# Kernel optimization log

Measured on AMD Instinct MI355X. Metric: run time of the kernel, lower is better.

## Reference

```python
import jax, jax.numpy as jnp
import numpy as np

G, FO, FI = 8, 64, 64   # n_group, fo, fi
N_ITER = 3
B, H, W = 32, 64, 64


def setup_inputs() -> dict:
    key = jax.random.key(0)
    k1, k2, k3 = jax.random.split(key, 3)
    x = jax.random.normal(k1, (B, G * FI, H, W), jnp.float32)
    # kaiming_normal on [fo*g, fi, 1, 1] -> std = sqrt(2/fi); stored as [g, fo, fi]
    weight = jax.random.normal(k2, (G, FO, FI), jnp.float32) * np.float32(np.sqrt(2.0 / FI))
    bias = jax.random.normal(k3, (FO,), jnp.float32)
    return {"x": x, "weight": weight, "bias": bias}


def reference(x, weight, bias):
    b, c, h, w = x.shape
    g, fo, fi = weight.shape
    # grouped 1x1 conv: split channels into g groups of fi, contract each with its [fo, fi] block
    xr = x.reshape(b, g, fi, h, w)
    con = jnp.einsum('bgihw,goi->bgohw', xr, weight)  # [B, g, fo, H, W]
    beta = jnp.zeros((1, g, 1, 1, 1), dtype=x.dtype)
    for i in range(N_ITER):
        alpha = jax.nn.sigmoid(beta)
        v = jnp.sum(alpha * con, axis=1, keepdims=True)      # [B, 1, fo, H, W]
        if i == N_ITER - 1:
            return v[:, 0] + bias[None, :, None, None]       # [B, fo, H, W]
        beta = beta + jnp.sum(v * con, axis=2, keepdims=True)  # [B, g, 1, H, W]
```

## Files before the change

### kernel.cpp

```cpp
#include <hip/hip_runtime.h>


#define NG 8
#define NFO 64
#define NFI 64
#define NB 32
#define NH 64
#define NW 64
#define HW (NH * NW)

typedef float v2f __attribute__((ext_vector_type(2)));

__device__ __forceinline__ void stage_piece(const float* gsrc, float* ldst) {
    __builtin_amdgcn_global_load_lds(
        (const __attribute__((address_space(1))) void*)gsrc,
        (__attribute__((address_space(3))) void*)ldst, 16, 0, 0);
}

__global__ __launch_bounds__(256) void dynrout_kernel(
    const float* __restrict__ x, const float* __restrict__ weight,
    const float* __restrict__ bias, float* __restrict__ out)
{
    const int tid = threadIdx.x;
    const int p = tid & 63;
    const int q = __builtin_amdgcn_readfirstlane(tid >> 6);

    const int wg = blockIdx.x;
    const int b = wg >> 6;
    const int h = wg & 63;

    __shared__ __align__(16) float smem[6144];

    const float* xrow = x + (size_t)b * (NG * NFI) * HW + (size_t)h * NW;
    const float* gpiece = xrow + (size_t)(p >> 4) * HW + (size_t)(p & 15) * 4;

    float con[8][16];
#pragma unroll
    for (int g = 0; g < 8; ++g)
#pragma unroll
        for (int f = 0; f < 16; ++f) con[g][f] = 0.f;

#pragma unroll
    for (int cc = 0; cc < 2; ++cc) {
        float* dst = smem + cc * 2048;
        const float* g0 = gpiece + (size_t)(cc * 32) * HW;
        stage_piece(g0 + (size_t)(q * 8) * HW,     dst + (q * 2) * 256);
        stage_piece(g0 + (size_t)(q * 8 + 4) * HW, dst + (q * 2 + 1) * 256);
    }

#pragma unroll
    for (int c = 0; c < 16; ++c) {
        if (c < 15) asm volatile("s_waitcnt vmcnt(2)" ::: "memory");
        else        asm volatile("s_waitcnt vmcnt(0)" ::: "memory");
        __builtin_amdgcn_s_barrier();

        if (c < 14) {
            float* dst = smem + ((c + 2) % 3) * 2048;
            const float* g0 = gpiece + (size_t)((c + 2) * 32) * HW;
            stage_piece(g0 + (size_t)(q * 8) * HW,     dst + (q * 2) * 256);
            stage_piece(g0 + (size_t)(q * 8 + 4) * HW, dst + (q * 2 + 1) * 256);
        }

        const int g = c >> 1;
        const float* bufp = smem + (c % 3) * 2048;

        v2f xp[16];
#pragma unroll
        for (int jp = 0; jp < 16; ++jp) {
            xp[jp].x = bufp[(2 * jp) * 64 + p];
            xp[jp].y = bufp[(2 * jp + 1) * 64 + p];
        }

        const float* wq = weight + ((size_t)g * NFO + (size_t)q * 16) * NFI + (c & 1) * 32;
#pragma unroll
        for (int f = 0; f < 16; ++f) {
            const float* wr = wq + (size_t)f * NFI;
            v2f a0 = {0.f, 0.f}, a1 = {0.f, 0.f};
#pragma unroll
            for (int jp = 0; jp < 16; jp += 2) {
                const v2f w0 = *(const v2f*)(wr + 2 * jp);
                const v2f w1 = *(const v2f*)(wr + 2 * jp + 2);
                a0 = __builtin_elementwise_fma(w0, xp[jp], a0);
                a1 = __builtin_elementwise_fma(w1, xp[jp + 1], a1);
            }
            con[g][f] += (a0.x + a1.x) + (a0.y + a1.y);
        }
    }
    __syncthreads();

    float* pbuf   = smem;
    float* alphaS = smem + 2048;
    float* betaS  = smem + 2560;

    float v[16];

#pragma unroll
    for (int f = 0; f < 16; ++f) {
        float s = con[0][f];
#pragma unroll
        for (int g = 1; g < 8; ++g) s += con[g][f];
        v[f] = 0.5f * s;
    }
#pragma unroll
    for (int g = 0; g < 8; ++g) {
        float s = 0.f;
#pragma unroll
        for (int f = 0; f < 16; ++f) s = fmaf(v[f], con[g][f], s);
        pbuf[(q * 8 + g) * 64 + p] = s;
    }
    __syncthreads();
    for (int k = tid; k < 512; k += 256) {
        const int gg = k >> 6, pp = k & 63;
        const float bs = pbuf[gg * 64 + pp] + pbuf[512 + gg * 64 + pp] +
                         pbuf[1024 + gg * 64 + pp] + pbuf[1536 + gg * 64 + pp];
        betaS[gg * 64 + pp] = bs;
        alphaS[gg * 64 + pp] = 1.f / (1.f + __expf(-bs));
    }
    __syncthreads();

    float a[8];
#pragma unroll
    for (int g = 0; g < 8; ++g) a[g] = alphaS[g * 64 + p];
#pragma unroll
    for (int f = 0; f < 16; ++f) {
        float s = 0.f;
#pragma unroll
        for (int g = 0; g < 8; ++g) s = fmaf(a[g], con[g][f], s);
        v[f] = s;
    }
#pragma unroll
    for (int g = 0; g < 8; ++g) {
        float s = 0.f;
#pragma unroll
        for (int f = 0; f < 16; ++f) s = fmaf(v[f], con[g][f], s);
        pbuf[(q * 8 + g) * 64 + p] = s;
    }
    __syncthreads();
    for (int k = tid; k < 512; k += 256) {
        const int gg = k >> 6, pp = k & 63;
        const float bs = betaS[gg * 64 + pp] +
                         pbuf[gg * 64 + pp] + pbuf[512 + gg * 64 + pp] +
                         pbuf[1024 + gg * 64 + pp] + pbuf[1536 + gg * 64 + pp];
        alphaS[gg * 64 + pp] = 1.f / (1.f + __expf(-bs));
    }
    __syncthreads();

#pragma unroll
    for (int g = 0; g < 8; ++g) a[g] = alphaS[g * 64 + p];

    const float* bq = bias + q * 16;
    float* orow = out + (((size_t)b * NFO + (size_t)q * 16) * NH + h) * NW + p;
#pragma unroll
    for (int f = 0; f < 16; ++f) {
        float s = bq[f];
#pragma unroll
        for (int g = 0; g < 8; ++g) s = fmaf(a[g], con[g][f], s);
        orow[(size_t)f * HW] = s;
    }
}

extern "C" void kernel_launch(void* const* d_in, const int* in_sizes, int n_in,
                              void* d_out, int out_size, void* d_ws, size_t ws_size,
                              hipStream_t stream) {
    const float* x      = (const float*)d_in[0];
    const float* weight = (const float*)d_in[1];
    const float* bias   = (const float*)d_in[2];
    float* out = (float*)d_out;

    dynrout_kernel<<<dim3(NB * NH), dim3(256), 0, stream>>>(x, weight, bias, out);
}
```

Before: 564.1 us.

## Split fused kernel into grouped-conv kernel and routing kernel via workspace

```diff
diff --git a/kernel.cpp b/kernel.cpp
--- a/kernel.cpp
+++ b/kernel.cpp
@@ -17,6 +17,155 @@
         (__attribute__((address_space(3))) void*)ldst, 16, 0, 0);
 }
 
+__global__ __launch_bounds__(256, 8) void conv_kernel(
+    const float* __restrict__ x, const float* __restrict__ weight,
+    float* __restrict__ con)
+{
+    const int tid = threadIdx.x;
+    const int p = tid & 63;
+    const int q = __builtin_amdgcn_readfirstlane(tid >> 6);
+
+    const int id = blockIdx.x;
+    const int t = id & 63;
+    const int g = (id >> 6) & 7;
+    const int b = id >> 9;
+
+    __shared__ __align__(16) float smem[4096];
+
+    const float* xg = x + ((size_t)b * (NG * NFI) + (size_t)g * NFI) * HW + t * 64;
+
+#pragma unroll
+    for (int cc = 0; cc < 4; ++cc) {
+        const int chb = q * 16 + cc * 4;
+        stage_piece(xg + (size_t)(chb + (p >> 4)) * HW + (p & 15) * 4,
+                    smem + chb * 64);
+    }
+    asm volatile("s_waitcnt vmcnt(0)" ::: "memory");
+    __builtin_amdgcn_s_barrier();
+
+    v2f acc[16];
+#pragma unroll
+    for (int f = 0; f < 16; ++f) acc[f] = (v2f){0.f, 0.f};
+
+    const float* wq = weight + ((size_t)g * NFO + (size_t)q * 16) * NFI;
+#pragma unroll
+    for (int ib = 0; ib < 8; ++ib) {
+        v2f xq[4];
+#pragma unroll
+        for (int j = 0; j < 4; ++j) {
+            xq[j].x = smem[(ib * 8 + 2 * j) * 64 + p];
+            xq[j].y = smem[(ib * 8 + 2 * j + 1) * 64 + p];
+        }
+#pragma unroll
+        for (int f = 0; f < 16; ++f) {
+            const float* wr = wq + (size_t)f * NFI + ib * 8;
+#pragma unroll
+            for (int j = 0; j < 4; ++j) {
+                const v2f wv = *(const v2f*)(wr + 2 * j);
+                acc[f] = __builtin_elementwise_fma(wv, xq[j], acc[f]);
+            }
+        }
+    }
+
+    float* crow = con + (((size_t)(b * NG + g) * NFO + (size_t)q * 16)) * HW
+                      + t * 64 + p;
+#pragma unroll
+    for (int f = 0; f < 16; ++f)
+        crow[(size_t)f * HW] = acc[f].x + acc[f].y;
+}
+
+__global__ __launch_bounds__(256) void route_kernel(
+    const float* __restrict__ con, const float* __restrict__ bias,
+    float* __restrict__ out)
+{
+    const int tid = threadIdx.x;
+    const int p = tid & 63;
+    const int q = __builtin_amdgcn_readfirstlane(tid >> 6);
+
+    const int id = blockIdx.x;
+    const int t = id & 63;
+    const int b = id >> 6;
+
+    __shared__ float pbuf[4][8][64];
+    __shared__ float alphaS[8][64];
+    __shared__ float betaS[8][64];
+
+    float c[8][16];
+#pragma unroll
+    for (int g = 0; g < 8; ++g) {
+        const float* cr = con + (((size_t)(b * NG + g) * NFO + (size_t)q * 16)) * HW
+                              + t * 64 + p;
+#pragma unroll
+        for (int f = 0; f < 16; ++f) c[g][f] = cr[(size_t)f * HW];
+    }
+
+    float v[16];
+
+#pragma unroll
+    for (int f = 0; f < 16; ++f) {
+        float s = c[0][f];
+#pragma unroll
+        for (int g = 1; g < 8; ++g) s += c[g][f];
+        v[f] = 0.5f * s;
+    }
+#pragma unroll
+    for (int g = 0; g < 8; ++g) {
+        float s = 0.f;
+#pragma unroll
+        for (int f = 0; f < 16; ++f) s = fmaf(v[f], c[g][f], s);
+        pbuf[q][g][p] = s;
+    }
+    __syncthreads();
+    for (int k = tid; k < 512; k += 256) {
+        const int gg = k >> 6, pp = k & 63;
+        const float bs = pbuf[0][gg][pp] + pbuf[1][gg][pp] +
+                         pbuf[2][gg][pp] + pbuf[3][gg][pp];
+        betaS[gg][pp] = bs;
+        alphaS[gg][pp] = 1.f / (1.f + __expf(-bs));
+    }
+    __syncthreads();
+
+    float a[8];
+#pragma unroll
+    for (int g = 0; g < 8; ++g) a[g] = alphaS[g][p];
+#pragma unroll
+    for (int f = 0; f < 16; ++f) {
+        float s = 0.f;
+#pragma unroll
+        for (int g = 0; g < 8; ++g) s = fmaf(a[g], c[g][f], s);
+        v[f] = s;
+    }
+#pragma unroll
+    for (int g = 0; g < 8; ++g) {
+        float s = 0.f;
+#pragma unroll
+        for (int f = 0; f < 16; ++f) s = fmaf(v[f], c[g][f], s);
+        pbuf[q][g][p] = s;
+    }
+    __syncthreads();
+    for (int k = tid; k < 512; k += 256) {
+        const int gg = k >> 6, pp = k & 63;
+        const float bs = betaS[gg][pp] +
+                         pbuf[0][gg][pp] + pbuf[1][gg][pp] +
+                         pbuf[2][gg][pp] + pbuf[3][gg][pp];
+        alphaS[gg][pp] = 1.f / (1.f + __expf(-bs));
+    }
+    __syncthreads();
+
+#pragma unroll
+    for (int g = 0; g < 8; ++g) a[g] = alphaS[g][p];
+
+    const float* bq = bias + q * 16;
+    float* orow = out + (((size_t)b * NFO + (size_t)q * 16) * NH + t) * NW + p;
+#pragma unroll
+    for (int f = 0; f < 16; ++f) {
+        float s = bq[f];
+#pragma unroll
+        for (int g = 0; g < 8; ++g) s = fmaf(a[g], c[g][f], s);
+        orow[(size_t)f * HW] = s;
+    }
+}
+
 __global__ __launch_bounds__(256) void dynrout_kernel(
     const float* __restrict__ x, const float* __restrict__ weight,
     const float* __restrict__ bias, float* __restrict__ out)
@@ -93,7 +242,6 @@
     float* betaS  = smem + 2560;
 
     float v[16];
-
 #pragma unroll
     for (int f = 0; f < 16; ++f) {
         float s = con[0][f];
@@ -167,5 +315,12 @@
     const float* bias   = (const float*)d_in[2];
     float* out = (float*)d_out;
 
-    dynrout_kernel<<<dim3(NB * NH), dim3(256), 0, stream>>>(x, weight, bias, out);
-}
+    const size_t need = (size_t)NB * NG * NFO * HW * sizeof(float);
+    if (d_ws != nullptr && ws_size >= need) {
+        float* con = (float*)d_ws;
+        conv_kernel<<<dim3(NB * NG * 64), dim3(256), 0, stream>>>(x, weight, con);
+        route_kernel<<<dim3(NB * 64), dim3(256), 0, stream>>>(con, bias, out);
+    } else {
+        dynrout_kernel<<<dim3(NB * NH), dim3(256), 0, stream>>>(x, weight, bias, out);
+    }
+}
```

Measured after the change: 491.3 us. -12.9%, faster.
